# Performance work log

Measured on AMD Instinct MI355X. Metric: run time of the kernel, lower is better.

## Reference

```python
import jax, jax.numpy as jnp
import numpy as np
from jax import lax


def _conv2d(x, w, pad=1):
    # x: (N,C,H,W), w: (O,I,kh,kw) -> (N,O,H,W)
    return lax.conv_general_dilated(
        x, w, window_strides=(1, 1), padding=[(pad, pad), (pad, pad)],
        dimension_numbers=("NCHW", "OIHW", "NCHW"))


def setup_inputs() -> dict:
    key = jax.random.key(0)
    ks = jax.random.split(key, 5)
    B, T, C, H, W = 4, 8, 256, 64, 64
    DH = 128
    fan = C * 3 * 3
    x = jax.random.normal(ks[0], (B, T, C, H, W), dtype=jnp.float32)
    w_k = jax.random.normal(ks[1], (DH, C, 3, 3), dtype=jnp.float32) * (2.0 / fan) ** 0.5
    w_q = jax.random.normal(ks[2], (DH, C, 3, 3), dtype=jnp.float32) * (2.0 / fan) ** 0.5
    w_v = jax.random.normal(ks[3], (DH, C, 3, 3), dtype=jnp.float32) * (2.0 / fan) ** 0.5
    w_out = jax.random.normal(ks[4], (C, DH, 3, 3), dtype=jnp.float32) * (2.0 / (DH * 9)) ** 0.5
    b_out = jnp.zeros((C,), dtype=jnp.float32)
    return {"x": x, "w_k": w_k, "w_q": w_q, "w_v": w_v, "w_out": w_out, "b_out": b_out}


def reference(x, w_k, w_q, w_v, w_out, b_out):
    B, T, C, H, W = x.shape
    DH = w_k.shape[0]
    # key comes only from the first frame
    k = _conv2d(x[:, 0], w_k)                                  # (B,DH,H,W)
    xf = x.reshape(B * T, C, H, W)
    q = _conv2d(xf, w_q).reshape(B, T, DH, H, W)               # (B,T,DH,H,W)
    v = _conv2d(xf, w_v).reshape(B, T, DH, H, W)
    # per-pixel channel dot between each frame's q and the single k
    dots = jnp.einsum("btchw,bchw->bthw", q, k)                # (B,T,H,W)
    attn = jax.nn.softmax(dots, axis=1)                        # softmax over T
    pooled = jnp.einsum("bthw,btchw->bchw", attn, v)           # (B,DH,H,W)
    # out conv applied once (result is identical for every repeated frame)
    out = _conv2d(pooled, w_out) + b_out[None, :, None, None]  # (B,C,H,W)
    return jnp.broadcast_to(out[:, None], (B, T, C, H, W))
```

## Files before the change

kernel.cpp:

```cpp
#include <hip/hip_runtime.h>
#include <cstdint>
#include <cstddef>

#define NB 4
#define NT 8
#define NC 256
#define NDH 128
#define HWs 4096

typedef _Float16 f16;
typedef _Float16 f16x8 __attribute__((ext_vector_type(8)));
typedef float f32x16 __attribute__((ext_vector_type(16)));


__global__ __launch_bounds__(256) void prep_x_kernel(const float* __restrict__ x,
                                                     f16* __restrict__ xh) {
    __shared__ f16 sxt[256 * 66];
    int bt = blockIdx.x >> 6, h = blockIdx.x & 63;
    int tid = threadIdx.x;
    int w = tid & 63, c4 = tid >> 6;
    for (int p = 0; p < 64; ++p) {
        int c = p * 4 + c4;
        sxt[c * 66 + w] = (f16)x[(((size_t)bt * NC + c) * 64 + h) * 64 + w];
    }
    __syncthreads();
    int cg = tid & 31, wb = tid >> 5;
    f16x8* xh8 = (f16x8*)xh;
    for (int p = 0; p < 8; ++p) {
        int w2 = wb * 8 + p;
        f16x8 v;
        #pragma unroll
        for (int j = 0; j < 8; ++j) v[j] = sxt[(cg * 8 + j) * 66 + w2];
        xh8[((size_t)(bt * 64 + h) * 64 + w2) * 32 + cg] = v;
    }
}

__global__ __launch_bounds__(256) void prep_w_kernel(const float* __restrict__ w,
                                                     f16* __restrict__ wt2,
                                                     int OC, int CIN) {
    int CG = CIN >> 3;
    int idx = blockIdx.x * 256 + threadIdx.x;
    if (idx >= OC * CG) return;
    int oc = idx / CG, cg = idx - oc * CG;
    f16x8* wt8 = (f16x8*)wt2;
    #pragma unroll
    for (int tap = 0; tap < 9; ++tap) {
        f16x8 v;
        #pragma unroll
        for (int j = 0; j < 8; ++j)
            v[j] = (f16)w[((size_t)oc * CIN + cg * 8 + j) * 9 + tap];
        wt8[((size_t)tap * CG + cg) * OC + oc] = v;
    }
}

template <int CIN>
__device__ __forceinline__ void conv_core(const f16x8* __restrict__ xh8,
                                          const f16x8* __restrict__ wt8,
                                          int OCT, int oc0, int h0,
                                          f16x8* __restrict__ sx8,
                                          f16x8* __restrict__ sw8,
                                          f32x16 acc[4][2]) {
    const int tid = threadIdx.x;
    const int lane = tid & 63;
    const int wv = tid >> 6;
    const int n = lane & 31, q = lane >> 5;
    const int CG = CIN / 8;

    #pragma unroll
    for (int i = 0; i < 4; ++i)
        #pragma unroll
        for (int ct = 0; ct < 2; ++ct)
            #pragma unroll
            for (int r = 0; r < 16; ++r) acc[i][ct][r] = 0.0f;

    f16x8 Z8 = {(f16)0, (f16)0, (f16)0, (f16)0, (f16)0, (f16)0, (f16)0, (f16)0};

    for (int c0 = 0; c0 < CIN; c0 += 16) {
        const int cg0 = c0 >> 3;
        __syncthreads();
        for (int j = wv; j < 36; j += 4) {
            int tap = j >> 2, qh = (j >> 1) & 1, hf = j & 1;
            int oc = hf * 64 + lane;
            sw8[(tap * 2 + qh) * 128 + oc] =
                wt8[(size_t)(tap * CG + cg0 + qh) * OCT + oc0 + oc];
        }
        for (int r = wv; r < 6; r += 4) {
            int h = h0 - 1 + r;
            if ((unsigned)h < 64u) {
                #pragma unroll
                for (int cb = 0; cb < 2; ++cb) {
                    int col = cb * 32 + (lane >> 1);
                    int sl = lane & 1;
                    int cidx = col + 1;
                    int cg = cg0 + (sl ^ ((cidx >> 2) & 1));
                    sx8[r * 132 + cidx * 2 + sl] = xh8[(size_t)(h * 64 + col) * CG + cg];
                }
                if (lane < 4)
                    sx8[r * 132 + (lane >> 1) * 130 + (lane & 1)] = Z8;
            } else {
                sx8[r * 132 + lane] = Z8;
                sx8[r * 132 + 64 + lane] = Z8;
                if (lane < 4) sx8[r * 132 + 128 + lane] = Z8;
            }
        }
        __syncthreads();
        #pragma unroll
        for (int tap = 0; tap < 9; ++tap) {
            const int ky = tap / 3, kx = tap % 3;
            f16x8 a[4];
            #pragma unroll
            for (int i = 0; i < 4; ++i)
                a[i] = sw8[(tap * 2 + q) * 128 + 32 * i + n];
            #pragma unroll
            for (int ct = 0; ct < 2; ++ct) {
                int cidx = ct * 32 + n + kx;
                int s = q ^ ((cidx >> 2) & 1);
                f16x8 b = sx8[(wv + ky) * 132 + cidx * 2 + s];
                #pragma unroll
                for (int i = 0; i < 4; ++i)
                    acc[i][ct] = __builtin_amdgcn_mfma_f32_32x32x16_f16(a[i], b, acc[i][ct], 0, 0, 0);
            }
        }
    }
}

__global__ __launch_bounds__(256, 2) void conv_k_kernel(const f16* __restrict__ xh,
        const f16* __restrict__ wk2, float* __restrict__ kbuf) {
    __shared__ f16x8 sx8[6 * 132];
    __shared__ f16x8 sw8[9 * 2 * 128];
    int b = blockIdx.x >> 4, hb = blockIdx.x & 15;
    int h0 = hb * 4;
    int bt = b * NT;
    f32x16 acc[4][2];
    conv_core<NC>((const f16x8*)xh + (size_t)bt * 64 * 64 * 32, (const f16x8*)wk2,
                  NDH, 0, h0, sx8, sw8, acc);
    int lane = threadIdx.x & 63, wv = threadIdx.x >> 6;
    int n = lane & 31, q = lane >> 5;
    int h = h0 + wv;
    #pragma unroll
    for (int i = 0; i < 4; ++i)
        #pragma unroll
        for (int r = 0; r < 16; ++r) {
            int oc = 32 * i + 4 * q + (r & 3) + 8 * (r >> 2);
            float* kp = kbuf + ((size_t)(b * NDH + oc)) * HWs + h * 64;
            kp[n] = acc[i][0][r];
            kp[32 + n] = acc[i][1][r];
        }
}

__global__ __launch_bounds__(256, 2) void conv_q_kernel(const f16* __restrict__ xh,
        const f16* __restrict__ wq2, const float* __restrict__ kbuf,
        float* __restrict__ dots) {
    __shared__ f16x8 sx8[6 * 132];
    __shared__ f16x8 sw8[9 * 2 * 128];
    int bt = blockIdx.x >> 4, hb = blockIdx.x & 15;
    int b = bt >> 3;
    int h0 = hb * 4;
    f32x16 acc[4][2];
    conv_core<NC>((const f16x8*)xh + (size_t)bt * 64 * 64 * 32, (const f16x8*)wq2,
                  NDH, 0, h0, sx8, sw8, acc);
    int lane = threadIdx.x & 63, wv = threadIdx.x >> 6;
    int n = lane & 31, q = lane >> 5;
    int h = h0 + wv;
    float p0 = 0.0f, p1 = 0.0f;
    #pragma unroll
    for (int i = 0; i < 4; ++i)
        #pragma unroll
        for (int r = 0; r < 16; ++r) {
            int oc = 32 * i + 4 * q + (r & 3) + 8 * (r >> 2);
            const float* kp = kbuf + ((size_t)(b * NDH + oc)) * HWs + h * 64;
            p0 += acc[i][0][r] * kp[n];
            p1 += acc[i][1][r] * kp[32 + n];
        }
    p0 += __shfl_xor(p0, 32, 64);
    p1 += __shfl_xor(p1, 32, 64);
    if (q == 0) {
        dots[(size_t)bt * HWs + h * 64 + n] = p0;
        dots[(size_t)bt * HWs + h * 64 + 32 + n] = p1;
    }
}

__global__ __launch_bounds__(256) void softmax_t_kernel(float* __restrict__ dots) {
    int idx = blockIdx.x * 256 + threadIdx.x;
    int b = idx >> 12;
    int p = idx & 4095;
    float* base = dots + (size_t)b * NT * HWs + p;
    float v[NT];
    float m = -3.4e38f;
    #pragma unroll
    for (int t = 0; t < NT; ++t) { v[t] = base[t * HWs]; m = fmaxf(m, v[t]); }
    float s = 0.0f;
    #pragma unroll
    for (int t = 0; t < NT; ++t) { v[t] = __expf(v[t] - m); s += v[t]; }
    float inv = 1.0f / s;
    #pragma unroll
    for (int t = 0; t < NT; ++t) base[t * HWs] = v[t] * inv;
}

__global__ __launch_bounds__(256, 2) void conv_v_kernel(const f16* __restrict__ xh,
        const f16* __restrict__ wv2, const float* __restrict__ attn,
        f16* __restrict__ parts) {
    __shared__ f16x8 sx8[6 * 132];
    __shared__ f16x8 sw8[9 * 2 * 128];
    int bt = blockIdx.x >> 4, hb = blockIdx.x & 15;
    int b = bt >> 3, t = bt & 7;
    int h0 = hb * 4;
    f32x16 acc[4][2];
    conv_core<NC>((const f16x8*)xh + (size_t)bt * 64 * 64 * 32, (const f16x8*)wv2,
                  NDH, 0, h0, sx8, sw8, acc);
    int lane = threadIdx.x & 63, wv = threadIdx.x >> 6;
    int n = lane & 31, q = lane >> 5;
    int h = h0 + wv;
    float a0 = attn[(size_t)bt * HWs + h * 64 + n];
    float a1 = attn[(size_t)bt * HWs + h * 64 + 32 + n];
    f16* pp = parts + (size_t)(t * NB + b) * NDH * HWs;
    #pragma unroll
    for (int i = 0; i < 4; ++i)
        #pragma unroll
        for (int r = 0; r < 16; ++r) {
            int oc = 32 * i + 4 * q + (r & 3) + 8 * (r >> 2);
            f16* op = pp + (size_t)oc * HWs + h * 64;
            op[n] = (f16)(a0 * acc[i][0][r]);
            op[32 + n] = (f16)(a1 * acc[i][1][r]);
        }
}

__global__ __launch_bounds__(256) void prep_pooled_kernel(const f16* __restrict__ parts,
                                                          f16* __restrict__ pooledT) {
    __shared__ f16 sxt[128 * 66];
    int b = blockIdx.x >> 6, h = blockIdx.x & 63;
    int tid = threadIdx.x, w = tid & 63, c4 = tid >> 6;
    for (int p = 0; p < 32; ++p) {
        int c = p * 4 + c4;
        float s = 0.0f;
        #pragma unroll
        for (int t = 0; t < NT; ++t)
            s += (float)parts[(((size_t)(t * NB + b) * NDH + c)) * HWs + h * 64 + w];
        sxt[c * 66 + w] = (f16)s;
    }
    __syncthreads();
    int cg = tid & 15, wb = tid >> 4;
    f16x8* pt8 = (f16x8*)pooledT;
    for (int p = 0; p < 4; ++p) {
        int w2 = wb * 4 + p;
        f16x8 v;
        #pragma unroll
        for (int j = 0; j < 8; ++j) v[j] = sxt[(cg * 8 + j) * 66 + w2];
        pt8[((size_t)(b * 64 + h) * 64 + w2) * 16 + cg] = v;
    }
}

__global__ __launch_bounds__(256, 2) void conv_out_kernel(const f16* __restrict__ pooledT,
        const f16* __restrict__ wo2, const float* __restrict__ b_out,
        float* __restrict__ out) {
    __shared__ f16x8 sx8[6 * 132];
    __shared__ f16x8 sw8[9 * 2 * 128];
    int b = blockIdx.x >> 5, oh = (blockIdx.x >> 4) & 1, hb = blockIdx.x & 15;
    int h0 = hb * 4;
    f32x16 acc[4][2];
    conv_core<NDH>((const f16x8*)pooledT + (size_t)b * 64 * 64 * 16, (const f16x8*)wo2,
                   NC, oh * 128, h0, sx8, sw8, acc);
    int lane = threadIdx.x & 63, wv = threadIdx.x >> 6;
    int n = lane & 31, q = lane >> 5;
    int h = h0 + wv;
    #pragma unroll
    for (int i = 0; i < 4; ++i)
        #pragma unroll
        for (int r = 0; r < 16; ++r) {
            int oc = oh * 128 + 32 * i + 4 * q + (r & 3) + 8 * (r >> 2);
            float bias = b_out[oc];
            float v0 = acc[i][0][r] + bias;
            float v1 = acc[i][1][r] + bias;
            for (int t = 0; t < NT; ++t) {
                float* op = out + ((size_t)(b * NT + t) * NC + oc) * HWs + h * 64;
                op[n] = v0;
                op[32 + n] = v1;
            }
        }
}

extern "C" void kernel_launch(void* const* d_in, const int* in_sizes, int n_in,
                              void* d_out, int out_size, void* d_ws, size_t ws_size,
                              hipStream_t stream) {
    (void)in_sizes; (void)n_in; (void)out_size; (void)ws_size;
    const float* x     = (const float*)d_in[0];
    const float* w_k   = (const float*)d_in[1];
    const float* w_q   = (const float*)d_in[2];
    const float* w_v   = (const float*)d_in[3];
    const float* w_out = (const float*)d_in[4];
    const float* b_out = (const float*)d_in[5];
    float* out = (float*)d_out;

    char* ws = (char*)d_ws;
    f16*   xh      = (f16*)ws;
    float* kbuf    = (float*)(ws + 67108864);
    float* dots    = (float*)(ws + 75497472);
    f16*   parts   = (f16*)(ws + 76021760);
    f16*   pooledT = (f16*)(ws + 109576192);
    f16*   wq2     = (f16*)(ws + 113770496);
    f16*   wk2     = (f16*)(ws + 114360320);
    f16*   wv2     = (f16*)(ws + 114950144);
    f16*   wo2     = (f16*)(ws + 115539968);

    hipLaunchKernelGGL(prep_x_kernel, dim3(2048), dim3(256), 0, stream, x, xh);
    hipLaunchKernelGGL(prep_w_kernel, dim3(16), dim3(256), 0, stream, w_q, wq2, NDH, NC);
    hipLaunchKernelGGL(prep_w_kernel, dim3(16), dim3(256), 0, stream, w_k, wk2, NDH, NC);
    hipLaunchKernelGGL(prep_w_kernel, dim3(16), dim3(256), 0, stream, w_v, wv2, NDH, NC);
    hipLaunchKernelGGL(prep_w_kernel, dim3(16), dim3(256), 0, stream, w_out, wo2, NC, NDH);

    hipLaunchKernelGGL(conv_k_kernel, dim3(NB * 16), dim3(256), 0, stream, xh, wk2, kbuf);
    hipLaunchKernelGGL(conv_q_kernel, dim3(NB * NT * 16), dim3(256), 0, stream, xh, wq2, kbuf, dots);
    hipLaunchKernelGGL(softmax_t_kernel, dim3(64), dim3(256), 0, stream, dots);
    hipLaunchKernelGGL(conv_v_kernel, dim3(NB * NT * 16), dim3(256), 0, stream, xh, wv2, dots, parts);
    hipLaunchKernelGGL(prep_pooled_kernel, dim3(256), dim3(256), 0, stream, parts, pooledT);
    hipLaunchKernelGGL(conv_out_kernel, dim3(NB * 16 * 2), dim3(256), 0, stream, pooledT, wo2, b_out, out);
}
```

Baseline: 555.0 us.

## Double-buffer conv tiles with direct global-to-LDS loads and retile 64oc×8rows

Restructures the shared conv core to double-buffer input and weight tiles in LDS. Loads go through global_load_lds so the next channel chunk is staged while MFMAs run on the current one. The block tile changes from 128 output channels × 4 rows to 64 channels × 8 rows, which splits the q-dot reduction into two per-channel-half partials that the softmax kernel now sums. This is meant to hide load latency and halve syncs per chunk, at the cost of more LDS per block and an extra partial buffer that aliases the parts workspace.

```diff
diff --git a/kernel.cpp b/kernel.cpp
--- a/kernel.cpp
+++ b/kernel.cpp
@@ -12,6 +12,12 @@
 typedef _Float16 f16x8 __attribute__((ext_vector_type(8)));
 typedef float f32x16 __attribute__((ext_vector_type(16)));
 
+
+__device__ __forceinline__ void gload16(const void* g, void* l) {
+    __builtin_amdgcn_global_load_lds(
+        (const __attribute__((address_space(1))) void*)g,
+        (__attribute__((address_space(3))) void*)l, 16, 0, 0);
+}
 
 __global__ __launch_bounds__(256) void prep_x_kernel(const float* __restrict__ x,
                                                      f16* __restrict__ xh) {
@@ -54,145 +60,175 @@
 }
 
 template <int CIN>
-__device__ __forceinline__ void conv_core(const f16x8* __restrict__ xh8,
-                                          const f16x8* __restrict__ wt8,
-                                          int OCT, int oc0, int h0,
-                                          f16x8* __restrict__ sx8,
-                                          f16x8* __restrict__ sw8,
-                                          f32x16 acc[4][2]) {
+__device__ __forceinline__ void conv_core2(const f16x8* __restrict__ xh8,
+                                           const f16x8* __restrict__ wt8,
+                                           int OCT, int oc0, int h0,
+                                           f16x8* __restrict__ sxb,
+                                           f16x8* __restrict__ swb,
+                                           f32x16 acc[2][2][2]) {
     const int tid = threadIdx.x;
     const int lane = tid & 63;
     const int wv = tid >> 6;
     const int n = lane & 31, q = lane >> 5;
     const int CG = CIN / 8;
-
-    #pragma unroll
-    for (int i = 0; i < 4; ++i)
-        #pragma unroll
-        for (int ct = 0; ct < 2; ++ct)
-            #pragma unroll
-            for (int r = 0; r < 16; ++r) acc[i][ct][r] = 0.0f;
+    const int NI = CIN / 16;
+
+    #pragma unroll
+    for (int oi = 0; oi < 2; ++oi)
+        #pragma unroll
+        for (int rr = 0; rr < 2; ++rr)
+            #pragma unroll
+            for (int ct = 0; ct < 2; ++ct)
+                #pragma unroll
+                for (int r = 0; r < 16; ++r) acc[oi][rr][ct][r] = 0.0f;
 
     f16x8 Z8 = {(f16)0, (f16)0, (f16)0, (f16)0, (f16)0, (f16)0, (f16)0, (f16)0};
 
-    for (int c0 = 0; c0 < CIN; c0 += 16) {
-        const int cg0 = c0 >> 3;
-        __syncthreads();
-        for (int j = wv; j < 36; j += 4) {
-            int tap = j >> 2, qh = (j >> 1) & 1, hf = j & 1;
-            int oc = hf * 64 + lane;
-            sw8[(tap * 2 + qh) * 128 + oc] =
-                wt8[(size_t)(tap * CG + cg0 + qh) * OCT + oc0 + oc];
-        }
-        for (int r = wv; r < 6; r += 4) {
+    #pragma unroll
+    for (int bufi = 0; bufi < 2; ++bufi) {
+        f16x8* sx8 = sxb + bufi * 1320;
+        if (tid < 40) {
+            int r = tid >> 2, k = tid & 3;
+            sx8[r * 132 + (k >> 1) * 130 + (k & 1)] = Z8;
+        }
+        for (int r = 0; r < 10; ++r) {
+            int h = h0 - 1 + r;
+            if ((unsigned)h >= 64u && tid < 132) sx8[r * 132 + tid] = Z8;
+        }
+    }
+
+    auto stage = [&](f16x8* sx8, f16x8* sw8, int cg0) {
+        for (int j = wv; j < 18; j += 4) {
+            int tap = j >> 1, qh = j & 1;
+            gload16(wt8 + (size_t)(tap * CG + cg0 + qh) * OCT + oc0 + lane,
+                    sw8 + (tap * 2 + qh) * 64);
+        }
+        for (int j = wv; j < 20; j += 4) {
+            int r = j >> 1, cb = j & 1;
             int h = h0 - 1 + r;
             if ((unsigned)h < 64u) {
-                #pragma unroll
-                for (int cb = 0; cb < 2; ++cb) {
-                    int col = cb * 32 + (lane >> 1);
-                    int sl = lane & 1;
-                    int cidx = col + 1;
-                    int cg = cg0 + (sl ^ ((cidx >> 2) & 1));
-                    sx8[r * 132 + cidx * 2 + sl] = xh8[(size_t)(h * 64 + col) * CG + cg];
-                }
-                if (lane < 4)
-                    sx8[r * 132 + (lane >> 1) * 130 + (lane & 1)] = Z8;
-            } else {
-                sx8[r * 132 + lane] = Z8;
-                sx8[r * 132 + 64 + lane] = Z8;
-                if (lane < 4) sx8[r * 132 + 128 + lane] = Z8;
-            }
-        }
-        __syncthreads();
+                int col = cb * 32 + (lane >> 1);
+                int cidx = col + 1;
+                int cg = cg0 + ((lane & 1) ^ ((cidx >> 2) & 1));
+                gload16(xh8 + (size_t)(h * 64 + col) * CG + cg,
+                        sx8 + r * 132 + 2 + cb * 64);
+            }
+        }
+    };
+
+    stage(sxb, swb, 0);
+    asm volatile("s_waitcnt vmcnt(0)" ::: "memory");
+    __syncthreads();
+
+    for (int it = 0; it < NI; ++it) {
+        f16x8* sx8 = sxb + (it & 1) * 1320;
+        f16x8* sw8 = swb + (it & 1) * 1152;
+        if (it + 1 < NI)
+            stage(sxb + ((it + 1) & 1) * 1320, swb + ((it + 1) & 1) * 1152,
+                  (it + 1) * 2);
         #pragma unroll
         for (int tap = 0; tap < 9; ++tap) {
             const int ky = tap / 3, kx = tap % 3;
-            f16x8 a[4];
-            #pragma unroll
-            for (int i = 0; i < 4; ++i)
-                a[i] = sw8[(tap * 2 + q) * 128 + 32 * i + n];
-            #pragma unroll
-            for (int ct = 0; ct < 2; ++ct) {
-                int cidx = ct * 32 + n + kx;
-                int s = q ^ ((cidx >> 2) & 1);
-                f16x8 b = sx8[(wv + ky) * 132 + cidx * 2 + s];
+            f16x8 a0 = sw8[(tap * 2 + q) * 64 + n];
+            f16x8 a1 = sw8[(tap * 2 + q) * 64 + 32 + n];
+            #pragma unroll
+            for (int rr = 0; rr < 2; ++rr) {
+                const int r = wv * 2 + rr + ky;
                 #pragma unroll
-                for (int i = 0; i < 4; ++i)
-                    acc[i][ct] = __builtin_amdgcn_mfma_f32_32x32x16_f16(a[i], b, acc[i][ct], 0, 0, 0);
-            }
-        }
+                for (int ct = 0; ct < 2; ++ct) {
+                    int cidx = ct * 32 + n + kx;
+                    int s = q ^ ((cidx >> 2) & 1);
+                    f16x8 b = sx8[r * 132 + cidx * 2 + s];
+                    acc[0][rr][ct] = __builtin_amdgcn_mfma_f32_32x32x16_f16(a0, b, acc[0][rr][ct], 0, 0, 0);
+                    acc[1][rr][ct] = __builtin_amdgcn_mfma_f32_32x32x16_f16(a1, b, acc[1][rr][ct], 0, 0, 0);
+                }
+            }
+        }
+        asm volatile("s_waitcnt vmcnt(0)" ::: "memory");
+        __syncthreads();
     }
 }
 
 __global__ __launch_bounds__(256, 2) void conv_k_kernel(const f16* __restrict__ xh,
         const f16* __restrict__ wk2, float* __restrict__ kbuf) {
-    __shared__ f16x8 sx8[6 * 132];
-    __shared__ f16x8 sw8[9 * 2 * 128];
-    int b = blockIdx.x >> 4, hb = blockIdx.x & 15;
-    int h0 = hb * 4;
+    __shared__ f16x8 sxb[2640];
+    __shared__ f16x8 swb[2304];
+    int bx = blockIdx.x;
+    int b = bx >> 4, ocg = (bx >> 3) & 1, hb = bx & 7;
+    int h0 = hb * 8, oc0 = ocg * 64;
     int bt = b * NT;
-    f32x16 acc[4][2];
-    conv_core<NC>((const f16x8*)xh + (size_t)bt * 64 * 64 * 32, (const f16x8*)wk2,
-                  NDH, 0, h0, sx8, sw8, acc);
+    f32x16 acc[2][2][2];
+    conv_core2<NC>((const f16x8*)xh + (size_t)bt * 64 * 64 * 32, (const f16x8*)wk2,
+                   NDH, oc0, h0, sxb, swb, acc);
     int lane = threadIdx.x & 63, wv = threadIdx.x >> 6;
     int n = lane & 31, q = lane >> 5;
-    int h = h0 + wv;
-    #pragma unroll
-    for (int i = 0; i < 4; ++i)
-        #pragma unroll
-        for (int r = 0; r < 16; ++r) {
-            int oc = 32 * i + 4 * q + (r & 3) + 8 * (r >> 2);
-            float* kp = kbuf + ((size_t)(b * NDH + oc)) * HWs + h * 64;
-            kp[n] = acc[i][0][r];
-            kp[32 + n] = acc[i][1][r];
-        }
+    #pragma unroll
+    for (int rr = 0; rr < 2; ++rr) {
+        int h = h0 + wv * 2 + rr;
+        #pragma unroll
+        for (int oi = 0; oi < 2; ++oi)
+            #pragma unroll
+            for (int r = 0; r < 16; ++r) {
+                int oc = oc0 + oi * 32 + 4 * q + (r & 3) + 8 * (r >> 2);
+                float* kp = kbuf + ((size_t)(b * NDH + oc)) * HWs + h * 64;
+                kp[n] = acc[oi][rr][0][r];
+                kp[32 + n] = acc[oi][rr][1][r];
+            }
+    }
 }
 
 __global__ __launch_bounds__(256, 2) void conv_q_kernel(const f16* __restrict__ xh,
         const f16* __restrict__ wq2, const float* __restrict__ kbuf,
-        float* __restrict__ dots) {
-    __shared__ f16x8 sx8[6 * 132];
-    __shared__ f16x8 sw8[9 * 2 * 128];
-    int bt = blockIdx.x >> 4, hb = blockIdx.x & 15;
+        float* __restrict__ qpart) {
+    __shared__ f16x8 sxb[2640];
+    __shared__ f16x8 swb[2304];
+    int bx = blockIdx.x;
+    int bt = bx >> 4, ocg = (bx >> 3) & 1, hb = bx & 7;
     int b = bt >> 3;
-    int h0 = hb * 4;
-    f32x16 acc[4][2];
-    conv_core<NC>((const f16x8*)xh + (size_t)bt * 64 * 64 * 32, (const f16x8*)wq2,
-                  NDH, 0, h0, sx8, sw8, acc);
+    int h0 = hb * 8, oc0 = ocg * 64;
+    f32x16 acc[2][2][2];
+    conv_core2<NC>((const f16x8*)xh + (size_t)bt * 64 * 64 * 32, (const f16x8*)wq2,
+                   NDH, oc0, h0, sxb, swb, acc);
     int lane = threadIdx.x & 63, wv = threadIdx.x >> 6;
     int n = lane & 31, q = lane >> 5;
-    int h = h0 + wv;
-    float p0 = 0.0f, p1 = 0.0f;
-    #pragma unroll
-    for (int i = 0; i < 4; ++i)
-        #pragma unroll
-        for (int r = 0; r < 16; ++r) {
-            int oc = 32 * i + 4 * q + (r & 3) + 8 * (r >> 2);
-            const float* kp = kbuf + ((size_t)(b * NDH + oc)) * HWs + h * 64;
-            p0 += acc[i][0][r] * kp[n];
-            p1 += acc[i][1][r] * kp[32 + n];
-        }
-    p0 += __shfl_xor(p0, 32, 64);
-    p1 += __shfl_xor(p1, 32, 64);
-    if (q == 0) {
-        dots[(size_t)bt * HWs + h * 64 + n] = p0;
-        dots[(size_t)bt * HWs + h * 64 + 32 + n] = p1;
-    }
-}
-
-__global__ __launch_bounds__(256) void softmax_t_kernel(float* __restrict__ dots) {
+    #pragma unroll
+    for (int rr = 0; rr < 2; ++rr) {
+        int h = h0 + wv * 2 + rr;
+        float p0 = 0.0f, p1 = 0.0f;
+        #pragma unroll
+        for (int oi = 0; oi < 2; ++oi)
+            #pragma unroll
+            for (int r = 0; r < 16; ++r) {
+                int oc = oc0 + oi * 32 + 4 * q + (r & 3) + 8 * (r >> 2);
+                const float* kp = kbuf + ((size_t)(b * NDH + oc)) * HWs + h * 64;
+                p0 += acc[oi][rr][0][r] * kp[n];
+                p1 += acc[oi][rr][1][r] * kp[32 + n];
+            }
+        p0 += __shfl_xor(p0, 32, 64);
+        p1 += __shfl_xor(p1, 32, 64);
+        if (q == 0) {
+            qpart[((size_t)ocg * 32 + bt) * HWs + h * 64 + n] = p0;
+            qpart[((size_t)ocg * 32 + bt) * HWs + h * 64 + 32 + n] = p1;
+        }
+    }
+}
+
+__global__ __launch_bounds__(256) void softmax_t_kernel(const float* __restrict__ qpart,
+                                                        float* __restrict__ dots) {
     int idx = blockIdx.x * 256 + threadIdx.x;
     int b = idx >> 12;
     int p = idx & 4095;
-    float* base = dots + (size_t)b * NT * HWs + p;
+    const float* q0 = qpart + (size_t)(b * NT) * HWs + p;
+    const float* q1 = qpart + (size_t)(32 + b * NT) * HWs + p;
     float v[NT];
     float m = -3.4e38f;
     #pragma unroll
-    for (int t = 0; t < NT; ++t) { v[t] = base[t * HWs]; m = fmaxf(m, v[t]); }
+    for (int t = 0; t < NT; ++t) { v[t] = q0[t * HWs] + q1[t * HWs]; m = fmaxf(m, v[t]); }
     float s = 0.0f;
     #pragma unroll
     for (int t = 0; t < NT; ++t) { v[t] = __expf(v[t] - m); s += v[t]; }
     float inv = 1.0f / s;
+    float* base = dots + (size_t)b * NT * HWs + p;
     #pragma unroll
     for (int t = 0; t < NT; ++t) base[t * HWs] = v[t] * inv;
 }
@@ -200,29 +236,33 @@
 __global__ __launch_bounds__(256, 2) void conv_v_kernel(const f16* __restrict__ xh,
         const f16* __restrict__ wv2, const float* __restrict__ attn,
         f16* __restrict__ parts) {
-    __shared__ f16x8 sx8[6 * 132];
-    __shared__ f16x8 sw8[9 * 2 * 128];
-    int bt = blockIdx.x >> 4, hb = blockIdx.x & 15;
+    __shared__ f16x8 sxb[2640];
+    __shared__ f16x8 swb[2304];
+    int bx = blockIdx.x;
+    int bt = bx >> 4, ocg = (bx >> 3) & 1, hb = bx & 7;
     int b = bt >> 3, t = bt & 7;
-    int h0 = hb * 4;
-    f32x16 acc[4][2];
-    conv_core<NC>((const f16x8*)xh + (size_t)bt * 64 * 64 * 32, (const f16x8*)wv2,
-                  NDH, 0, h0, sx8, sw8, acc);
+    int h0 = hb * 8, oc0 = ocg * 64;
+    f32x16 acc[2][2][2];
+    conv_core2<NC>((const f16x8*)xh + (size_t)bt * 64 * 64 * 32, (const f16x8*)wv2,
+                   NDH, oc0, h0, sxb, swb, acc);
     int lane = threadIdx.x & 63, wv = threadIdx.x >> 6;
     int n = lane & 31, q = lane >> 5;
-    int h = h0 + wv;
-    float a0 = attn[(size_t)bt * HWs + h * 64 + n];
-    float a1 = attn[(size_t)bt * HWs + h * 64 + 32 + n];
     f16* pp = parts + (size_t)(t * NB + b) * NDH * HWs;
     #pragma unroll
-    for (int i = 0; i < 4; ++i)
-        #pragma unroll
-        for (int r = 0; r < 16; ++r) {
-            int oc = 32 * i + 4 * q + (r & 3) + 8 * (r >> 2);
-            f16* op = pp + (size_t)oc * HWs + h * 64;
-            op[n] = (f16)(a0 * acc[i][0][r]);
-            op[32 + n] = (f16)(a1 * acc[i][1][r]);
-        }
+    for (int rr = 0; rr < 2; ++rr) {
+        int h = h0 + wv * 2 + rr;
+        float a0 = attn[(size_t)bt * HWs + h * 64 + n];
+        float a1 = attn[(size_t)bt * HWs + h * 64 + 32 + n];
+        #pragma unroll
+        for (int oi = 0; oi < 2; ++oi)
+            #pragma unroll
+            for (int r = 0; r < 16; ++r) {
+                int oc = oc0 + oi * 32 + 4 * q + (r & 3) + 8 * (r >> 2);
+                f16* op = pp + (size_t)oc * HWs + h * 64;
+                op[n] = (f16)(a0 * acc[oi][rr][0][r]);
+                op[32 + n] = (f16)(a1 * acc[oi][rr][1][r]);
+            }
+    }
 }
 
 __global__ __launch_bounds__(256) void prep_pooled_kernel(const f16* __restrict__ parts,
@@ -253,30 +293,34 @@
 __global__ __launch_bounds__(256, 2) void conv_out_kernel(const f16* __restrict__ pooledT,
         const f16* __restrict__ wo2, const float* __restrict__ b_out,
         float* __restrict__ out) {
-    __shared__ f16x8 sx8[6 * 132];
-    __shared__ f16x8 sw8[9 * 2 * 128];
-    int b = blockIdx.x >> 5, oh = (blockIdx.x >> 4) & 1, hb = blockIdx.x & 15;
-    int h0 = hb * 4;
-    f32x16 acc[4][2];
-    conv_core<NDH>((const f16x8*)pooledT + (size_t)b * 64 * 64 * 16, (const f16x8*)wo2,
-                   NC, oh * 128, h0, sx8, sw8, acc);
+    __shared__ f16x8 sxb[2640];
+    __shared__ f16x8 swb[2304];
+    int bx = blockIdx.x;
+    int b = bx >> 5, ocg = (bx >> 3) & 3, hb = bx & 7;
+    int h0 = hb * 8, oc0 = ocg * 64;
+    f32x16 acc[2][2][2];
+    conv_core2<NDH>((const f16x8*)pooledT + (size_t)b * 64 * 64 * 16, (const f16x8*)wo2,
+                    NC, oc0, h0, sxb, swb, acc);
     int lane = threadIdx.x & 63, wv = threadIdx.x >> 6;
     int n = lane & 31, q = lane >> 5;
-    int h = h0 + wv;
-    #pragma unroll
-    for (int i = 0; i < 4; ++i)
-        #pragma unroll
-        for (int r = 0; r < 16; ++r) {
-            int oc = oh * 128 + 32 * i + 4 * q + (r & 3) + 8 * (r >> 2);
-            float bias = b_out[oc];
-            float v0 = acc[i][0][r] + bias;
-            float v1 = acc[i][1][r] + bias;
-            for (int t = 0; t < NT; ++t) {
-                float* op = out + ((size_t)(b * NT + t) * NC + oc) * HWs + h * 64;
-                op[n] = v0;
-                op[32 + n] = v1;
-            }
-        }
+    #pragma unroll
+    for (int rr = 0; rr < 2; ++rr) {
+        int h = h0 + wv * 2 + rr;
+        #pragma unroll
+        for (int oi = 0; oi < 2; ++oi)
+            #pragma unroll
+            for (int r = 0; r < 16; ++r) {
+                int oc = oc0 + oi * 32 + 4 * q + (r & 3) + 8 * (r >> 2);
+                float bias = b_out[oc];
+                float v0 = acc[oi][rr][0][r] + bias;
+                float v1 = acc[oi][rr][1][r] + bias;
+                for (int t = 0; t < NT; ++t) {
+                    float* op = out + ((size_t)(b * NT + t) * NC + oc) * HWs + h * 64;
+                    op[n] = v0;
+                    op[32 + n] = v1;
+                }
+            }
+    }
 }
 
 extern "C" void kernel_launch(void* const* d_in, const int* in_sizes, int n_in,
@@ -296,6 +340,7 @@
     float* kbuf    = (float*)(ws + 67108864);
     float* dots    = (float*)(ws + 75497472);
     f16*   parts   = (f16*)(ws + 76021760);
+    float* qpart   = (float*)(ws + 76021760);
     f16*   pooledT = (f16*)(ws + 109576192);
     f16*   wq2     = (f16*)(ws + 113770496);
     f16*   wk2     = (f16*)(ws + 114360320);
@@ -308,10 +353,10 @@
     hipLaunchKernelGGL(prep_w_kernel, dim3(16), dim3(256), 0, stream, w_v, wv2, NDH, NC);
     hipLaunchKernelGGL(prep_w_kernel, dim3(16), dim3(256), 0, stream, w_out, wo2, NC, NDH);
 
-    hipLaunchKernelGGL(conv_k_kernel, dim3(NB * 16), dim3(256), 0, stream, xh, wk2, kbuf);
-    hipLaunchKernelGGL(conv_q_kernel, dim3(NB * NT * 16), dim3(256), 0, stream, xh, wq2, kbuf, dots);
-    hipLaunchKernelGGL(softmax_t_kernel, dim3(64), dim3(256), 0, stream, dots);
-    hipLaunchKernelGGL(conv_v_kernel, dim3(NB * NT * 16), dim3(256), 0, stream, xh, wv2, dots, parts);
+    hipLaunchKernelGGL(conv_k_kernel, dim3(NB * 2 * 8), dim3(256), 0, stream, xh, wk2, kbuf);
+    hipLaunchKernelGGL(conv_q_kernel, dim3(NB * NT * 2 * 8), dim3(256), 0, stream, xh, wq2, kbuf, qpart);
+    hipLaunchKernelGGL(softmax_t_kernel, dim3(64), dim3(256), 0, stream, qpart, dots);
+    hipLaunchKernelGGL(conv_v_kernel, dim3(NB * NT * 2 * 8), dim3(256), 0, stream, xh, wv2, dots, parts);
     hipLaunchKernelGGL(prep_pooled_kernel, dim3(256), dim3(256), 0, stream, parts, pooledT);
-    hipLaunchKernelGGL(conv_out_kernel, dim3(NB * 16 * 2), dim3(256), 0, stream, pooledT, wo2, b_out, out);
-}
+    hipLaunchKernelGGL(conv_out_kernel, dim3(NB * 4 * 8), dim3(256), 0, stream, pooledT, wo2, b_out, out);
+}
```

New measurement: 501.7 us. 9.6% less time.
